# Optimization experiments

Hardware: AMD Instinct MI355X
Metric: run time of the kernel (lower is better)

The kernel has to match this reference:

```python
import jax, jax.numpy as jnp
import numpy as np

N_EDGES = 1048576
N_CENTERS = 32768
N_SPECIES = 4
L_MAX = 3
N_BASIS = 12
N_MAX = 8
R_CUT = 5.0
NORM = 1.0 / np.sqrt(32.0)  # hypers['normalize'] = avg_num_neighbors = 32
SH_SPLITS = [0, 1, 4, 9, 16]  # cumulative offsets of (2l+1)


def real_sph_harm_lmax3(u):
    # u: [E,3] unit vectors; returns [E,16] real normalized spherical harmonics (sphericart order m=-l..l)
    x, y, z = u[:, 0], u[:, 1], u[:, 2]
    c0 = 0.5 * np.sqrt(1.0 / np.pi)
    c1 = np.sqrt(3.0 / (4.0 * np.pi))
    x2, y2, z2 = x * x, y * y, z * z
    sh = [
        jnp.full_like(x, c0),
        c1 * y, c1 * z, c1 * x,
        0.5 * np.sqrt(15.0 / np.pi) * x * y,
        0.5 * np.sqrt(15.0 / np.pi) * y * z,
        0.25 * np.sqrt(5.0 / np.pi) * (3.0 * z2 - 1.0),
        0.5 * np.sqrt(15.0 / np.pi) * x * z,
        0.25 * np.sqrt(15.0 / np.pi) * (x2 - y2),
        0.25 * np.sqrt(35.0 / (2.0 * np.pi)) * y * (3.0 * x2 - y2),
        0.5 * np.sqrt(105.0 / np.pi) * x * y * z,
        0.25 * np.sqrt(21.0 / (2.0 * np.pi)) * y * (5.0 * z2 - 1.0),
        0.25 * np.sqrt(7.0 / np.pi) * (5.0 * z2 * z - 3.0 * z),
        0.25 * np.sqrt(21.0 / (2.0 * np.pi)) * x * (5.0 * z2 - 1.0),
        0.25 * np.sqrt(105.0 / np.pi) * z * (x2 - y2),
        0.25 * np.sqrt(35.0 / (2.0 * np.pi)) * x * (x2 - y2),
    ]
    return jnp.stack(sh, axis=1)


def setup_inputs() -> dict:
    key = jax.random.key(0)
    k1, k2, k3, k4 = jax.random.split(key, 4)
    vectors = jax.random.normal(k1, (N_EDGES, 3), dtype=jnp.float32) * 1.5
    radial_weights = jax.random.normal(k2, (L_MAX + 1, N_BASIS, N_MAX), dtype=jnp.float32) * 0.1
    center_index = jax.random.randint(k3, (N_EDGES,), 0, N_CENTERS, dtype=jnp.int64)
    neighbor_species_index = jax.random.randint(k4, (N_EDGES,), 0, N_SPECIES, dtype=jnp.int64)
    return {"vectors": vectors, "radial_weights": radial_weights,
            "center_index": center_index, "neighbor_species_index": neighbor_species_index}


def reference(vectors, radial_weights, center_index, neighbor_species_index):
    # distances and unit vectors
    r = jnp.sqrt(jnp.sum(vectors * vectors, axis=-1) + 1e-12)  # [E]
    u = vectors / r[:, None]
    # smooth radial basis phi_n(r) = sin((n+1) pi r / r_cut)/r, normalized (LE-like)
    ns = jnp.arange(1, N_BASIS + 1, dtype=vectors.dtype)
    phi = jnp.sin(np.pi / R_CUT * r[:, None] * ns[None, :]) / r[:, None] * NORM  # [E, N_BASIS]
    sh = real_sph_harm_lmax3(u)  # [E,16]
    # scatter target: (center, neighbor_species) channel
    idx = center_index * N_SPECIES + neighbor_species_index  # [E]
    densities = []
    for l in range(L_MAX + 1):
        m_l = 2 * l + 1
        sh_l = jax.lax.slice_in_dim(sh, SH_SPLITS[l], SH_SPLITS[l + 1], axis=1)  # [E, 2l+1]
        rad_l = phi @ radial_weights[l]  # [E, N_MAX]
        edge_l = rad_l[:, None, :] * sh_l[:, :, None]  # [E, 2l+1, N_MAX] outer product
        dens = jax.ops.segment_sum(edge_l.reshape(edge_l.shape[0], -1), idx,
                                   num_segments=N_CENTERS * N_SPECIES)  # [N*S, m*n]
        dens = dens.reshape(N_CENTERS, N_SPECIES, m_l, N_MAX)
        dens = jnp.transpose(dens, (0, 2, 1, 3)).reshape(N_CENTERS, m_l, N_SPECIES * N_MAX)
        densities.append(dens)  # c^{a_i l}_{Ai, m, a_j n}
    # concatenate the per-l TensorMap blocks along the m axis -> [N, sum(2l+1), S*N_MAX]
    return jnp.concatenate(densities, axis=1)
```

## Files before the change

### kernel.cpp

```cpp
#include <hip/hip_runtime.h>
#include <math.h>

#define N_EDGES   1048576
#define N_BUCKET  1024
#define SEG_PER_B 128
#define N_BASIS   12
#define CAP       2048
#define HBLK      256
#define HEPB      (N_EDGES / HBLK)


#define WS_BLKHIST  0
#define WS_TOTALS   (HBLK * N_BUCKET * 4)
#define WS_OFFSETS  (WS_TOTALS + N_BUCKET * 4)
#define WS_RECORDS  (WS_OFFSETS + N_BUCKET * 4)
#define WS_NEEDED   (WS_RECORDS + N_EDGES * 4)

__device__ __forceinline__ void compute_edge(float x, float y, float z,
                                             float* __restrict__ ph,
                                             float* __restrict__ sh)
{
    const float r2    = fmaf(x, x, fmaf(y, y, z * z)) + 1e-12f;
    const float inv_r = rsqrtf(r2);
    const float r     = r2 * inv_r;
    x *= inv_r; y *= inv_r; z *= inv_r;

    const float t = 0.6283185307179586f * r;
    float s1, c1;
    __sincosf(t, &s1, &c1);
    const float twoc = 2.0f * c1;
    const float scale = 0.17677669529663687f * inv_r;
    float skm1 = 0.0f, sk = s1;
    #pragma unroll
    for (int b = 0; b < N_BASIS; ++b) {
        ph[b] = sk * scale;
        const float nxt = fmaf(twoc, sk, -skm1);
        skm1 = sk; sk = nxt;
    }

    const float x2 = x * x, y2 = y * y, z2 = z * z;
    sh[0]  = 0.28209479177387814f;
    sh[1]  = 0.4886025119029199f * y;
    sh[2]  = 0.4886025119029199f * z;
    sh[3]  = 0.4886025119029199f * x;
    sh[4]  = 1.0925484305920792f * x * y;
    sh[5]  = 1.0925484305920792f * y * z;
    sh[6]  = 0.31539156525252005f * (3.0f * z2 - 1.0f);
    sh[7]  = 1.0925484305920792f * x * z;
    sh[8]  = 0.5462742152960396f * (x2 - y2);
    sh[9]  = 0.5900435899266435f * y * (3.0f * x2 - y2);
    sh[10] = 2.890611442640554f  * x * y * z;
    sh[11] = 0.4570457994644658f * y * (5.0f * z2 - 1.0f);
    sh[12] = 0.3731763325901154f * (5.0f * z2 * z - 3.0f * z);
    sh[13] = 0.4570457994644658f * x * (5.0f * z2 - 1.0f);
    sh[14] = 1.445305721320277f  * z * (x2 - y2);
    sh[15] = 0.5900435899266435f * x * (x2 - y2);
}

__device__ __forceinline__ void flush_seg(const float* __restrict__ acc,
                                          int b, int sl, int n,
                                          float* __restrict__ out)
{
    const int seg = b * SEG_PER_B + sl;
    float* op = out + (size_t)(seg >> 2) * 512 + (seg & 3) * 8 + n;
    #pragma unroll
    for (int L = 0; L < 16; ++L) op[L * 32] = acc[L];
}

__global__ __launch_bounds__(256) void hist_kernel(
    const int* __restrict__ cidx, const int* __restrict__ sidx,
    int* __restrict__ blkhist)
{
    __shared__ int h[N_BUCKET];
    const int t = threadIdx.x;
    #pragma unroll
    for (int i = t; i < N_BUCKET; i += 256) h[i] = 0;
    __syncthreads();
    const int base = blockIdx.x * HEPB;
    #pragma unroll
    for (int k = 0; k < HEPB / 256; ++k) {
        const int e = base + k * 256 + t;
        const int seg = (cidx[e] << 2) | sidx[e];
        atomicAdd(&h[seg >> 7], 1);
    }
    __syncthreads();
    #pragma unroll
    for (int i = t; i < N_BUCKET; i += 256)
        blkhist[blockIdx.x * N_BUCKET + i] = h[i];
}

__global__ __launch_bounds__(64) void scanA_kernel(
    int* __restrict__ blkhist, int* __restrict__ totals)
{
    const int bkt = blockIdx.x * 64 + threadIdx.x;
    int run = 0;
    for (int blk = 0; blk < HBLK; ++blk) {
        const int v = blkhist[blk * N_BUCKET + bkt];
        blkhist[blk * N_BUCKET + bkt] = run;
        run += v;
    }
    totals[bkt] = run;
}

__global__ __launch_bounds__(1024) void scanB_kernel(
    const int* __restrict__ totals, int* __restrict__ offsets)
{
    __shared__ int tmp[N_BUCKET];
    const int t = threadIdx.x;
    const int orig = totals[t];
    tmp[t] = orig;
    __syncthreads();
    #pragma unroll
    for (int d = 1; d < N_BUCKET; d <<= 1) {
        const int v = (t >= d) ? tmp[t - d] : 0;
        __syncthreads();
        tmp[t] += v;
        __syncthreads();
    }
    offsets[t] = tmp[t] - orig;
}

__global__ __launch_bounds__(256) void partition_kernel(
    const int* __restrict__ cidx, const int* __restrict__ sidx,
    const int* __restrict__ blkhist, const int* __restrict__ offsets,
    unsigned int* __restrict__ records)
{
    __shared__ int bb[N_BUCKET];
    __shared__ int lcnt[N_BUCKET];
    const int t = threadIdx.x;
    #pragma unroll
    for (int i = t; i < N_BUCKET; i += 256) {
        bb[i] = offsets[i] + blkhist[blockIdx.x * N_BUCKET + i];
        lcnt[i] = 0;
    }
    __syncthreads();
    const int base = blockIdx.x * HEPB;
    #pragma unroll
    for (int k = 0; k < HEPB / 256; ++k) {
        const int e = base + k * 256 + t;
        const int seg = (cidx[e] << 2) | sidx[e];
        const int bkt = seg >> 7;
        const int r = atomicAdd(&lcnt[bkt], 1);
        records[bb[bkt] + r] = ((unsigned)(seg & 127) << 20) | (unsigned)e;
    }
}

__global__ __launch_bounds__(256) void compute_kernel(
    const unsigned int* __restrict__ sorted_rec,
    const int* __restrict__ offsets, const int* __restrict__ counts,
    const float* __restrict__ vectors,
    const float* __restrict__ rw,
    float* __restrict__ out)
{
    __shared__ float4 pay[CAP];
    __shared__ int shist[SEG_PER_B];
    __shared__ int soff[SEG_PER_B];
    __shared__ int scur[SEG_PER_B];

    const int t = threadIdx.x;
    const int b = blockIdx.x;
    const int n = t & 7;
    const int g = t >> 3;

    float Wn[4][N_BASIS];
    #pragma unroll
    for (int l = 0; l < 4; ++l)
        #pragma unroll
        for (int bb = 0; bb < N_BASIS; ++bb)
            Wn[l][bb] = rw[(l * N_BASIS + bb) * 8 + n];

    const int off = offsets[b];
    const int cnt = counts[b];

    if (cnt > CAP) {
        #pragma unroll 1
        for (int k = 0; k < 4; ++k) {
            const int sl = g * 4 + k;
            float acc[16];
            #pragma unroll
            for (int L = 0; L < 16; ++L) acc[L] = 0.0f;
            for (int j = 0; j < cnt; ++j) {
                const unsigned rec = sorted_rec[off + j];
                if ((int)(rec >> 20) != sl) continue;
                const int eid = rec & 0xFFFFF;
                float ph[N_BASIS], sh[16];
                compute_edge(vectors[3*eid], vectors[3*eid+1], vectors[3*eid+2], ph, sh);
                float rad[4];
                #pragma unroll
                for (int l = 0; l < 4; ++l) {
                    float a = 0.0f;
                    #pragma unroll
                    for (int bb = 0; bb < N_BASIS; ++bb)
                        a = fmaf(ph[bb], Wn[l][bb], a);
                    rad[l] = a;
                }
                #pragma unroll
                for (int L = 0; L < 16; ++L) {
                    const int l = (L == 0) ? 0 : (L < 4) ? 1 : (L < 9) ? 2 : 3;
                    acc[L] = fmaf(sh[L], rad[l], acc[L]);
                }
            }
            flush_seg(acc, b, sl, n, out);
        }
        return;
    }

    if (t < SEG_PER_B) shist[t] = 0;
    __syncthreads();

    unsigned recs[8];
    const int iters = (cnt + 255) >> 8;
    #pragma unroll
    for (int it = 0; it < 8; ++it) {
        const int i = it * 256 + t;
        if (it < iters && i < cnt) {
            recs[it] = sorted_rec[off + i];
            atomicAdd(&shist[recs[it] >> 20], 1);
        }
    }
    __syncthreads();

    if (t < SEG_PER_B) soff[t] = shist[t];
    __syncthreads();
    #pragma unroll
    for (int d = 1; d < SEG_PER_B; d <<= 1) {
        int v = 0;
        if (t >= d && t < SEG_PER_B) v = soff[t - d];
        __syncthreads();
        if (t < SEG_PER_B) soff[t] += v;
        __syncthreads();
    }
    if (t < SEG_PER_B) {
        const int ex = soff[t] - shist[t];
        soff[t] = ex;
        scur[t] = ex;
    }
    __syncthreads();

    #pragma unroll
    for (int it = 0; it < 8; ++it) {
        const int i = it * 256 + t;
        if (it < iters && i < cnt) {
            const unsigned rec = recs[it];
            const int sl  = rec >> 20;
            const int eid = rec & 0xFFFFF;
            const int r = atomicAdd(&scur[sl], 1);
            pay[r] = make_float4(vectors[3 * eid], vectors[3 * eid + 1],
                                 vectors[3 * eid + 2], __int_as_float(sl));
        }
    }
    __syncthreads();

    const int s0 = g * 4;
    const int js = soff[s0];
    const int je = (s0 + 4 < SEG_PER_B) ? soff[s0 + 4] : cnt;

    int cur = -1;
    float acc[16];
    #pragma unroll
    for (int L = 0; L < 16; ++L) acc[L] = 0.0f;

    for (int j = js; j < je; ++j) {
        const float4 v = pay[j];
        const int sl = __float_as_int(v.w);
        if (sl != cur) {
            if (cur >= 0) {
                flush_seg(acc, b, cur, n, out);
                #pragma unroll
                for (int L = 0; L < 16; ++L) acc[L] = 0.0f;
            }
            cur = sl;
        }
        float ph[N_BASIS], sh[16];
        compute_edge(v.x, v.y, v.z, ph, sh);
        float rad[4];
        #pragma unroll
        for (int l = 0; l < 4; ++l) {
            float a = 0.0f;
            #pragma unroll
            for (int bb = 0; bb < N_BASIS; ++bb)
                a = fmaf(ph[bb], Wn[l][bb], a);
            rad[l] = a;
        }
        #pragma unroll
        for (int L = 0; L < 16; ++L) {
            const int l = (L == 0) ? 0 : (L < 4) ? 1 : (L < 9) ? 2 : 3;
            acc[L] = fmaf(sh[L], rad[l], acc[L]);
        }
    }
    if (cur >= 0) flush_seg(acc, b, cur, n, out);

    #pragma unroll
    for (int k = 0; k < 4; ++k) {
        const int sl = s0 + k;
        if (shist[sl] == 0) {
            float z[16];
            #pragma unroll
            for (int L = 0; L < 16; ++L) z[L] = 0.0f;
            flush_seg(z, b, sl, n, out);
        }
    }
}

__global__ __launch_bounds__(256) void atomic_kernel(
    const float* __restrict__ vectors, const float* __restrict__ rw,
    const int* __restrict__ cidx, const int* __restrict__ sidx,
    float* __restrict__ out)
{
    const int e = blockIdx.x * 256 + threadIdx.x;
    if (e >= N_EDGES) return;
    float ph[N_BASIS], sh[16];
    compute_edge(vectors[3*e], vectors[3*e+1], vectors[3*e+2], ph, sh);
    float* op = out + (size_t)cidx[e] * 512 + sidx[e] * 8;
    for (int l = 0; l < 4; ++l) {
        const int L0 = l * l;
        const int ml = 2 * l + 1;
        for (int nn = 0; nn < 8; ++nn) {
            float rad = 0.0f;
            for (int bb = 0; bb < N_BASIS; ++bb)
                rad = fmaf(ph[bb], rw[(l * N_BASIS + bb) * 8 + nn], rad);
            for (int mm = 0; mm < ml; ++mm)
                atomicAdd(op + (L0 + mm) * 32 + nn, sh[L0 + mm] * rad);
        }
    }
}

extern "C" void kernel_launch(void* const* d_in, const int* in_sizes, int n_in,
                              void* d_out, int out_size, void* d_ws, size_t ws_size,
                              hipStream_t stream) {
    const float* vectors = (const float*)d_in[0];
    const float* rw      = (const float*)d_in[1];
    const int*   cidx    = (const int*)d_in[2];
    const int*   sidx    = (const int*)d_in[3];
    float*       out     = (float*)d_out;

    if (ws_size < (size_t)WS_NEEDED) {
        hipMemsetAsync(out, 0, (size_t)out_size * sizeof(float), stream);
        hipLaunchKernelGGL(atomic_kernel, dim3(N_EDGES / 256), dim3(256), 0, stream,
                           vectors, rw, cidx, sidx, out);
        return;
    }

    char* ws = (char*)d_ws;
    int*          blkhist = (int*)(ws + WS_BLKHIST);
    int*          totals  = (int*)(ws + WS_TOTALS);
    int*          offsets = (int*)(ws + WS_OFFSETS);
    unsigned int* records = (unsigned int*)(ws + WS_RECORDS);

    hipLaunchKernelGGL(hist_kernel,      dim3(HBLK),      dim3(256),  0, stream, cidx, sidx, blkhist);
    hipLaunchKernelGGL(scanA_kernel,     dim3(N_BUCKET/64), dim3(64), 0, stream, blkhist, totals);
    hipLaunchKernelGGL(scanB_kernel,     dim3(1),         dim3(1024), 0, stream, totals, offsets);
    hipLaunchKernelGGL(partition_kernel, dim3(HBLK),      dim3(256),  0, stream, cidx, sidx, blkhist, offsets, records);
    hipLaunchKernelGGL(compute_kernel,   dim3(N_BUCKET),  dim3(256),  0, stream, records, offsets, totals, vectors, rw, out);
}
```

Baseline: 169.9 us.

## Merge scan kernels, shrink histogram grid, and write segments branch-free in compute

Cuts the histogram and partition grids from 256 to 64 blocks of 1024 threads and fuses the two scan kernels into one single-block kernel, removing one launch and shrinking the per-block histogram table. The compute loop now processes its four segments in fixed pairs with two accumulators and always writes every segment, replacing the per-edge segment-change check and the separate zero-fill pass. The cost is less parallelism in the hist and partition passes, a serial 64-step loop in the scan, and more register pressure from the two accumulator sets.

```diff
diff --git a/kernel.cpp b/kernel.cpp
--- a/kernel.cpp
+++ b/kernel.cpp
@@ -6,7 +6,7 @@
 #define SEG_PER_B 128
 #define N_BASIS   12
 #define CAP       2048
-#define HBLK      256
+#define HBLK      64
 #define HEPB      (N_EDGES / HBLK)
 
 
@@ -57,6 +57,28 @@
     sh[15] = 0.5900435899266435f * x * (x2 - y2);
 }
 
+__device__ __forceinline__ void accum_edge(const float4 v,
+                                           const float (&Wn)[4][N_BASIS],
+                                           float* __restrict__ acc)
+{
+    float ph[N_BASIS], sh[16];
+    compute_edge(v.x, v.y, v.z, ph, sh);
+    float rad[4];
+    #pragma unroll
+    for (int l = 0; l < 4; ++l) {
+        float a = 0.0f;
+        #pragma unroll
+        for (int bb = 0; bb < N_BASIS; ++bb)
+            a = fmaf(ph[bb], Wn[l][bb], a);
+        rad[l] = a;
+    }
+    #pragma unroll
+    for (int L = 0; L < 16; ++L) {
+        const int l = (L == 0) ? 0 : (L < 4) ? 1 : (L < 9) ? 2 : 3;
+        acc[L] = fmaf(sh[L], rad[l], acc[L]);
+    }
+}
+
 __device__ __forceinline__ void flush_seg(const float* __restrict__ acc,
                                           int b, int sl, int n,
                                           float* __restrict__ out)
@@ -67,48 +89,39 @@
     for (int L = 0; L < 16; ++L) op[L * 32] = acc[L];
 }
 
-__global__ __launch_bounds__(256) void hist_kernel(
+__global__ __launch_bounds__(1024) void hist_kernel(
     const int* __restrict__ cidx, const int* __restrict__ sidx,
     int* __restrict__ blkhist)
 {
     __shared__ int h[N_BUCKET];
     const int t = threadIdx.x;
-    #pragma unroll
-    for (int i = t; i < N_BUCKET; i += 256) h[i] = 0;
+    h[t] = 0;
     __syncthreads();
     const int base = blockIdx.x * HEPB;
     #pragma unroll
-    for (int k = 0; k < HEPB / 256; ++k) {
-        const int e = base + k * 256 + t;
+    for (int k = 0; k < HEPB / 1024; ++k) {
+        const int e = base + k * 1024 + t;
         const int seg = (cidx[e] << 2) | sidx[e];
         atomicAdd(&h[seg >> 7], 1);
     }
     __syncthreads();
-    #pragma unroll
-    for (int i = t; i < N_BUCKET; i += 256)
-        blkhist[blockIdx.x * N_BUCKET + i] = h[i];
-}
-
-__global__ __launch_bounds__(64) void scanA_kernel(
-    int* __restrict__ blkhist, int* __restrict__ totals)
-{
-    const int bkt = blockIdx.x * 64 + threadIdx.x;
+    blkhist[blockIdx.x * N_BUCKET + t] = h[t];
+}
+
+__global__ __launch_bounds__(1024) void scan_kernel(
+    int* __restrict__ blkhist, int* __restrict__ totals,
+    int* __restrict__ offsets)
+{
+    __shared__ int tmp[N_BUCKET];
+    const int t = threadIdx.x;
     int run = 0;
     for (int blk = 0; blk < HBLK; ++blk) {
-        const int v = blkhist[blk * N_BUCKET + bkt];
-        blkhist[blk * N_BUCKET + bkt] = run;
+        const int v = blkhist[blk * N_BUCKET + t];
+        blkhist[blk * N_BUCKET + t] = run;
         run += v;
     }
-    totals[bkt] = run;
-}
-
-__global__ __launch_bounds__(1024) void scanB_kernel(
-    const int* __restrict__ totals, int* __restrict__ offsets)
-{
-    __shared__ int tmp[N_BUCKET];
-    const int t = threadIdx.x;
-    const int orig = totals[t];
-    tmp[t] = orig;
+    totals[t] = run;
+    tmp[t] = run;
     __syncthreads();
     #pragma unroll
     for (int d = 1; d < N_BUCKET; d <<= 1) {
@@ -117,10 +130,10 @@
         tmp[t] += v;
         __syncthreads();
     }
-    offsets[t] = tmp[t] - orig;
-}
-
-__global__ __launch_bounds__(256) void partition_kernel(
+    offsets[t] = tmp[t] - run;
+}
+
+__global__ __launch_bounds__(1024) void partition_kernel(
     const int* __restrict__ cidx, const int* __restrict__ sidx,
     const int* __restrict__ blkhist, const int* __restrict__ offsets,
     unsigned int* __restrict__ records)
@@ -128,16 +141,13 @@
     __shared__ int bb[N_BUCKET];
     __shared__ int lcnt[N_BUCKET];
     const int t = threadIdx.x;
-    #pragma unroll
-    for (int i = t; i < N_BUCKET; i += 256) {
-        bb[i] = offsets[i] + blkhist[blockIdx.x * N_BUCKET + i];
-        lcnt[i] = 0;
-    }
+    bb[t]   = offsets[t] + blkhist[blockIdx.x * N_BUCKET + t];
+    lcnt[t] = 0;
     __syncthreads();
     const int base = blockIdx.x * HEPB;
     #pragma unroll
-    for (int k = 0; k < HEPB / 256; ++k) {
-        const int e = base + k * 256 + t;
+    for (int k = 0; k < HEPB / 1024; ++k) {
+        const int e = base + k * 1024 + t;
         const int seg = (cidx[e] << 2) | sidx[e];
         const int bkt = seg >> 7;
         const int r = atomicAdd(&lcnt[bkt], 1);
@@ -145,32 +155,16 @@
     }
 }
 
-__global__ __launch_bounds__(256) void compute_kernel(
-    const unsigned int* __restrict__ sorted_rec,
-    const int* __restrict__ offsets, const int* __restrict__ counts,
-    const float* __restrict__ vectors,
-    const float* __restrict__ rw,
-    float* __restrict__ out)
-{
-    __shared__ float4 pay[CAP];
-    __shared__ int shist[SEG_PER_B];
-    __shared__ int soff[SEG_PER_B];
-    __shared__ int scur[SEG_PER_B];
-
-    const int t = threadIdx.x;
-    const int b = blockIdx.x;
+__device__ __forceinline__ void compute_bucket(
+    const unsigned int* __restrict__ sorted_rec, int off, int cnt, int b,
+    const float* __restrict__ vectors, const float (&Wn)[4][N_BASIS],
+    float* __restrict__ out,
+    float4* __restrict__ pay, int* __restrict__ shist,
+    int* __restrict__ soff, int* __restrict__ scur)
+{
+    const int t = threadIdx.x;
     const int n = t & 7;
     const int g = t >> 3;
-
-    float Wn[4][N_BASIS];
-    #pragma unroll
-    for (int l = 0; l < 4; ++l)
-        #pragma unroll
-        for (int bb = 0; bb < N_BASIS; ++bb)
-            Wn[l][bb] = rw[(l * N_BASIS + bb) * 8 + n];
-
-    const int off = offsets[b];
-    const int cnt = counts[b];
 
     if (cnt > CAP) {
         #pragma unroll 1
@@ -183,22 +177,9 @@
                 const unsigned rec = sorted_rec[off + j];
                 if ((int)(rec >> 20) != sl) continue;
                 const int eid = rec & 0xFFFFF;
-                float ph[N_BASIS], sh[16];
-                compute_edge(vectors[3*eid], vectors[3*eid+1], vectors[3*eid+2], ph, sh);
-                float rad[4];
-                #pragma unroll
-                for (int l = 0; l < 4; ++l) {
-                    float a = 0.0f;
-                    #pragma unroll
-                    for (int bb = 0; bb < N_BASIS; ++bb)
-                        a = fmaf(ph[bb], Wn[l][bb], a);
-                    rad[l] = a;
-                }
-                #pragma unroll
-                for (int L = 0; L < 16; ++L) {
-                    const int l = (L == 0) ? 0 : (L < 4) ? 1 : (L < 9) ? 2 : 3;
-                    acc[L] = fmaf(sh[L], rad[l], acc[L]);
-                }
+                const float4 v = make_float4(vectors[3*eid], vectors[3*eid+1],
+                                             vectors[3*eid+2], 0.0f);
+                accum_edge(v, Wn, acc);
             }
             flush_seg(acc, b, sl, n, out);
         }
@@ -251,55 +232,56 @@
     }
     __syncthreads();
 
+    float* ob = out + (size_t)(b * 32 + g) * 512 + n;
     const int s0 = g * 4;
-    const int js = soff[s0];
-    const int je = (s0 + 4 < SEG_PER_B) ? soff[s0 + 4] : cnt;
-
-    int cur = -1;
-    float acc[16];
-    #pragma unroll
-    for (int L = 0; L < 16; ++L) acc[L] = 0.0f;
-
-    for (int j = js; j < je; ++j) {
-        const float4 v = pay[j];
-        const int sl = __float_as_int(v.w);
-        if (sl != cur) {
-            if (cur >= 0) {
-                flush_seg(acc, b, cur, n, out);
-                #pragma unroll
-                for (int L = 0; L < 16; ++L) acc[L] = 0.0f;
-            }
-            cur = sl;
-        }
-        float ph[N_BASIS], sh[16];
-        compute_edge(v.x, v.y, v.z, ph, sh);
-        float rad[4];
+    #pragma unroll
+    for (int kp = 0; kp < 2; ++kp) {
+        float accA[16], accB[16];
         #pragma unroll
-        for (int l = 0; l < 4; ++l) {
-            float a = 0.0f;
-            #pragma unroll
-            for (int bb = 0; bb < N_BASIS; ++bb)
-                a = fmaf(ph[bb], Wn[l][bb], a);
-            rad[l] = a;
-        }
+        for (int L = 0; L < 16; ++L) { accA[L] = 0.0f; accB[L] = 0.0f; }
+
+        const int sA  = s0 + 2 * kp;
+        const int jsA = soff[sA];
+        const int jeA = soff[sA + 1];
+        for (int j = jsA; j < jeA; ++j) accum_edge(pay[j], Wn, accA);
+
+        const int sB  = sA + 1;
+        const int jsB = soff[sB];
+        const int jeB = (sB + 1 < SEG_PER_B) ? soff[sB + 1] : cnt;
+        for (int j = jsB; j < jeB; ++j) accum_edge(pay[j], Wn, accB);
+
         #pragma unroll
         for (int L = 0; L < 16; ++L) {
-            const int l = (L == 0) ? 0 : (L < 4) ? 1 : (L < 9) ? 2 : 3;
-            acc[L] = fmaf(sh[L], rad[l], acc[L]);
-        }
-    }
-    if (cur >= 0) flush_seg(acc, b, cur, n, out);
-
-    #pragma unroll
-    for (int k = 0; k < 4; ++k) {
-        const int sl = s0 + k;
-        if (shist[sl] == 0) {
-            float z[16];
-            #pragma unroll
-            for (int L = 0; L < 16; ++L) z[L] = 0.0f;
-            flush_seg(z, b, sl, n, out);
-        }
-    }
+            ob[L * 32 + (2 * kp) * 8]     = accA[L];
+            ob[L * 32 + (2 * kp) * 8 + 8] = accB[L];
+        }
+    }
+}
+
+__global__ __launch_bounds__(256) void compute_kernel(
+    const unsigned int* __restrict__ sorted_rec,
+    const int* __restrict__ offsets, const int* __restrict__ counts,
+    const float* __restrict__ vectors,
+    const float* __restrict__ rw, float* __restrict__ out)
+{
+    __shared__ float4 pay[CAP];
+    __shared__ int shist[SEG_PER_B];
+    __shared__ int soff[SEG_PER_B];
+    __shared__ int scur[SEG_PER_B];
+
+    const int t = threadIdx.x;
+    const int b = blockIdx.x;
+    const int n = t & 7;
+
+    float Wn[4][N_BASIS];
+    #pragma unroll
+    for (int l = 0; l < 4; ++l)
+        #pragma unroll
+        for (int bb = 0; bb < N_BASIS; ++bb)
+            Wn[l][bb] = rw[(l * N_BASIS + bb) * 8 + n];
+
+    compute_bucket(sorted_rec, offsets[b], counts[b], b, vectors, Wn, out,
+                   pay, shist, soff, scur);
 }
 
 __global__ __launch_bounds__(256) void atomic_kernel(
@@ -347,9 +329,8 @@
     int*          offsets = (int*)(ws + WS_OFFSETS);
     unsigned int* records = (unsigned int*)(ws + WS_RECORDS);
 
-    hipLaunchKernelGGL(hist_kernel,      dim3(HBLK),      dim3(256),  0, stream, cidx, sidx, blkhist);
-    hipLaunchKernelGGL(scanA_kernel,     dim3(N_BUCKET/64), dim3(64), 0, stream, blkhist, totals);
-    hipLaunchKernelGGL(scanB_kernel,     dim3(1),         dim3(1024), 0, stream, totals, offsets);
-    hipLaunchKernelGGL(partition_kernel, dim3(HBLK),      dim3(256),  0, stream, cidx, sidx, blkhist, offsets, records);
-    hipLaunchKernelGGL(compute_kernel,   dim3(N_BUCKET),  dim3(256),  0, stream, records, offsets, totals, vectors, rw, out);
-}
+    hipLaunchKernelGGL(hist_kernel,      dim3(HBLK),     dim3(1024), 0, stream, cidx, sidx, blkhist);
+    hipLaunchKernelGGL(scan_kernel,      dim3(1),        dim3(1024), 0, stream, blkhist, totals, offsets);
+    hipLaunchKernelGGL(partition_kernel, dim3(HBLK),     dim3(1024), 0, stream, cidx, sidx, blkhist, offsets, records);
+    hipLaunchKernelGGL(compute_kernel,   dim3(N_BUCKET), dim3(256),  0, stream, records, offsets, totals, vectors, rw, out);
+}
```

Result: no change. 172.8 us (+1.7%).
